# Optimization experiments

Measured on AMD Instinct MI355X. Metric: run time of the kernel, lower is better.

## Reference

```python
import jax, jax.numpy as jnp
import numpy as np

MASS, CHARGE, ALPHA, BETA = 1.0, 0.5, 0.1, 0.05
ETA = jnp.array([1.0, -1.0, -1.0, -1.0], dtype=jnp.float32)  # Minkowski metric diag


def setup_inputs() -> dict:
    key = jax.random.key(0)
    k1, k2, k3 = jax.random.split(key, 3)
    B = 262144
    y = jax.random.normal(k1, (B, 8), dtype=jnp.float32)
    W = jax.random.normal(k2, (4, 4), dtype=jnp.float32) * 0.3
    V = jax.random.normal(k3, (4, 4), dtype=jnp.float32) * 0.3
    return {"y": y, "W": W, "V": V}


def _lagrangian(z):
    # z = (x, u, A) concatenated, shape [12]
    x, u, A = z[0:4], z[4:8], z[8:12]
    kinetic = 0.5 * MASS * jnp.sum(ETA * u * u)
    coupling = CHARGE * jnp.sum(ETA * u * A)
    xu_term = ALPHA * jnp.sum((x * u) ** 2)      # makes J_xu nontrivial
    uA_term = BETA * jnp.sum(u * A) ** 2          # makes J_Au nontrivial
    return kinetic + coupling + xu_term + uA_term


def reference(y, W, V):
    def A_vec(x):  # vector potential A^mu(x), works on [4] or [B,4]
        return jnp.tanh(x @ W.T) + x @ V.T

    x = y[:, 0:4]   # [B,4] positions
    u = y[:, 4:8]   # [B,4] velocities
    A = A_vec(x)    # [B,4]
    z = jnp.concatenate([x, u, A], axis=1)  # [B,12] = (x,u,A)

    gradL = jax.vmap(jax.grad(_lagrangian))(z)      # [B,12]
    H = jax.vmap(jax.hessian(_lagrangian))(z)       # [B,12,12]

    dL_dx = gradL[:, 0:4]
    dL_dA = gradL[:, 8:12]
    J_xu = H[:, 0:4, 4:8]    # d^2L/(dx^mu du^nu)
    J_uu = H[:, 4:8, 4:8]    # d^2L/(du^mu du^nu)
    J_Au = H[:, 8:12, 4:8]   # d^2L/(dA^mu du^nu)

    # dA_dx[a, nu, i] = dA^i/dx^nu (matches tf.stack(..., axis=2) layout)
    jacA = jax.vmap(jax.jacfwd(A_vec))(x)           # [B, i, nu]
    dA_dx = jnp.transpose(jacA, (0, 2, 1))          # [B, nu, i]

    J_uu_inv = jnp.linalg.pinv(J_uu)                # [B,4,4]

    force = (dL_dx
             + jnp.einsum('ajk,ak->aj', dA_dx, dL_dA)
             - jnp.einsum('ai,aij->aj', u,
                          J_xu + jnp.einsum('ajk,akm->ajm', dA_dx, J_Au)))
    acceleration = jnp.einsum('ai,aij->aj', force, J_uu_inv)  # [B,4]
    return acceleration
```

## Files before the change

### kernel.cpp

```cpp
#include <hip/hip_runtime.h>
#include <math.h>


#define SIX_RCOND 2.86102294921875e-5
#define RCOND     4.76837158203125e-6

__device__ __forceinline__ float rcp_nr(float x) {
    float r = __builtin_amdgcn_rcpf(x);
    r = r * (2.0f - x * r);
    return r;
}

__device__ __forceinline__ void fast_tanh4(const double t[4], double th[4])
{
    const double LOG2E = 1.4426950408889634074;
    const double LN2HI = 6.93147180369123816490e-01;
    const double LN2LO = 1.90821492927058770002e-10;
    double e[4], opp[4];
    #pragma unroll
    for (int j = 0; j < 4; ++j) {
        double a  = fabs(t[j]);
        double z  = -2.0 * a;
        double zc = fmax(z, -64.0);
        double nf = rint(zc * LOG2E);
        double r  = fma(-nf, LN2HI, zc);
        r = fma(-nf, LN2LO, r);
        double p = 2.75573192239858906526e-07;
        p = fma(p, r, 2.75573192239858925110e-06);
        p = fma(p, r, 2.48015873015873015873e-05);
        p = fma(p, r, 1.98412698412698412698e-04);
        p = fma(p, r, 1.38888888888888888889e-03);
        p = fma(p, r, 8.33333333333333333333e-03);
        p = fma(p, r, 4.16666666666666666667e-02);
        p = fma(p, r, 1.66666666666666666667e-01);
        p = fma(p, r, 0.5);
        p = fma(p, r, 1.0);
        p = fma(p, r, 1.0);
        int n = (int)nf;
        double twon = __longlong_as_double(((long long)(1023 + n)) << 52);
        double ez = p * twon;
        ez = (z <= -40.0) ? 0.0 : ez;
        e[j]   = ez;
        opp[j] = 1.0 + ez;
    }
    double p01 = opp[0] * opp[1], p23 = opp[2] * opp[3];
    double rp  = 1.0 / (p01 * p23);
    double inv[4] = { opp[1] * p23 * rp, opp[0] * p23 * rp,
                      p01 * opp[3] * rp, p01 * opp[2] * rp };
    #pragma unroll
    for (int j = 0; j < 4; ++j)
        th[j] = copysign((1.0 - e[j]) * inv[j], t[j]);
}

__device__ __forceinline__ void model_terms_f64(
    const double* sW, const double* sV,
    const double x[4], const double u[4],
    double A[4], double f[4], double d[4])
{
    const double eta[4] = {1.0, -1.0, -1.0, -1.0};
    const double CHG = 0.5, ALPHA = 0.1, BETA = 0.05;
    double t[4], s[4];
    #pragma unroll
    for (int j = 0; j < 4; ++j) {
        double tj = 0.0, sj = 0.0;
        #pragma unroll
        for (int k = 0; k < 4; ++k) {
            tj = fma(sW[j*4+k], x[k], tj);
            sj = fma(sV[j*4+k], x[k], sj);
        }
        t[j] = tj; s[j] = sj;
    }
    double th[4];
    fast_tanh4(t, th);
    double G[4][4];
    #pragma unroll
    for (int j = 0; j < 4; ++j) {
        A[j] = th[j] + s[j];
        double dth = 1.0 - th[j] * th[j];
        #pragma unroll
        for (int k = 0; k < 4; ++k) G[j][k] = fma(dth, sW[j*4+k], sV[j*4+k]);
    }
    double S = 0.0;
    #pragma unroll
    for (int k = 0; k < 4; ++k) S += u[k] * A[k];
    double P[4], R[4], Q[4];
    #pragma unroll
    for (int j = 0; j < 4; ++j) {
        double p = 0.0, r = 0.0, q = 0.0;
        #pragma unroll
        for (int k = 0; k < 4; ++k) {
            p += G[k][j] * u[k];
            r += G[j][k] * u[k];
            q += G[k][j] * (CHG * eta[k]) * u[k];
        }
        P[j] = p; R[j] = r; Q[j] = q;
    }
    double T = 0.0;
    #pragma unroll
    for (int j = 0; j < 4; ++j) T += u[j] * R[j];
    #pragma unroll
    for (int j = 0; j < 4; ++j) {
        f[j] = -2.0 * ALPHA * x[j] * u[j] * u[j]
             + Q[j]
             + 2.0 * BETA * S * P[j]
             - (CHG * eta[j] + 2.0 * BETA * S) * R[j]
             - 2.0 * BETA * A[j] * T;
        d[j] = eta[j] + 2.0 * ALPHA * x[j] * x[j];
    }
}

__device__ __forceinline__ void sm_solve_f64(
    const double d[4], const double A[4], const double f[4], double acc[4])
{
    const double C2 = 0.1;
    double b[4], fd[4], den = 1.0, w = 0.0;
    #pragma unroll
    for (int j = 0; j < 4; ++j) {
        double inv = 1.0 / d[j];
        b[j]  = A[j] * inv;
        fd[j] = f[j] * inv;
        den  += C2 * A[j] * b[j];
        w    += b[j] * f[j];
    }
    double scale = C2 * w / den;
    #pragma unroll
    for (int j = 0; j < 4; ++j) acc[j] = fd[j] - b[j] * scale;
}

__device__ __forceinline__ void jacobi_pinv_solve(
    const double d[4], const double A[4], const double f[4], double acc[4])
{
    const double C2 = 0.1;
    double M[4][4], Vm[4][4];
    #pragma unroll
    for (int r = 0; r < 4; ++r) {
        #pragma unroll
        for (int c = 0; c < 4; ++c) {
            M[r][c] = C2 * A[r] * A[c];
            Vm[r][c] = (r == c) ? 1.0 : 0.0;
        }
        M[r][r] += d[r];
    }
    for (int sweep = 0; sweep < 8; ++sweep) {
        #pragma unroll
        for (int p = 0; p < 3; ++p) {
            #pragma unroll
            for (int q2 = p + 1; q2 < 4; ++q2) {
                double apq = M[p][q2];
                bool active = fabs(apq) > 1e-280;
                double div = active ? (2.0 * apq) : 1.0;
                double tau = (M[q2][q2] - M[p][p]) / div;
                double tt = ((tau >= 0.0) ? 1.0 : -1.0) /
                            (fabs(tau) + sqrt(1.0 + tau * tau));
                double c = 1.0 / sqrt(1.0 + tt * tt);
                double s = tt * c;
                c = active ? c : 1.0;
                s = active ? s : 0.0;
                #pragma unroll
                for (int k = 0; k < 4; ++k) {
                    double mkp = M[k][p], mkq = M[k][q2];
                    M[k][p]  = c * mkp - s * mkq;
                    M[k][q2] = s * mkp + c * mkq;
                }
                #pragma unroll
                for (int k = 0; k < 4; ++k) {
                    double mpk = M[p][k], mqk = M[q2][k];
                    M[p][k]  = c * mpk - s * mqk;
                    M[q2][k] = s * mpk + c * mqk;
                }
                #pragma unroll
                for (int k = 0; k < 4; ++k) {
                    double vkp = Vm[k][p], vkq = Vm[k][q2];
                    Vm[k][p]  = c * vkp - s * vkq;
                    Vm[k][q2] = s * vkp + c * vkq;
                }
            }
        }
    }
    double lam[4], sigmax = 0.0;
    #pragma unroll
    for (int k = 0; k < 4; ++k) {
        lam[k] = M[k][k];
        double a = fabs(lam[k]);
        sigmax = (a > sigmax) ? a : sigmax;
    }
    double cutoff = RCOND * sigmax;
    #pragma unroll
    for (int j = 0; j < 4; ++j) acc[j] = 0.0;
    #pragma unroll
    for (int e = 0; e < 4; ++e) {
        double coef = 0.0;
        #pragma unroll
        for (int k = 0; k < 4; ++k) coef += Vm[k][e] * f[k];
        coef /= lam[e];
        coef = (fabs(lam[e]) > cutoff) ? coef : 0.0;
        #pragma unroll
        for (int j = 0; j < 4; ++j) acc[j] += coef * Vm[j][e];
    }
}

__global__ __launch_bounds__(256) void fast_kernel(
    const float* __restrict__ y, const float* __restrict__ W,
    const float* __restrict__ V, float* __restrict__ out,
    unsigned int* __restrict__ cnt, int* __restrict__ list,
    unsigned int cap, int B)
{
    __shared__ float sW[16], sV[16];
    if (threadIdx.x < 16)      sW[threadIdx.x]      = W[threadIdx.x];
    else if (threadIdx.x < 32) sV[threadIdx.x - 16] = V[threadIdx.x - 16];
    __syncthreads();

    int i = blockIdx.x * blockDim.x + threadIdx.x;
    if (i >= B) return;

    const float4* y4 = (const float4*)y;
    float4 xv = y4[2 * i];
    float4 uv = y4[2 * i + 1];
    float x[4] = {xv.x, xv.y, xv.z, xv.w};
    float u[4] = {uv.x, uv.y, uv.z, uv.w};

    const float eta[4] = {1.0f, -1.0f, -1.0f, -1.0f};
    const float CHG = 0.5f, ALPHA = 0.1f, BETA = 0.05f, C2 = 0.1f;
    const float NEG2LOG2E = -2.8853900817779268f;

    float t[4], sv[4];
    #pragma unroll
    for (int j = 0; j < 4; ++j) {
        float tj = 0.0f, sj = 0.0f;
        #pragma unroll
        for (int k = 0; k < 4; ++k) {
            tj = fmaf(sW[j*4+k], x[k], tj);
            sj = fmaf(sV[j*4+k], x[k], sj);
        }
        t[j] = tj; sv[j] = sj;
    }
    float A[4], dth[4];
    #pragma unroll
    for (int j = 0; j < 4; ++j) {
        float a  = fabsf(t[j]);
        float e  = __builtin_amdgcn_exp2f(a * NEG2LOG2E);
        float th = copysignf((1.0f - e) * rcp_nr(1.0f + e), t[j]);
        A[j]   = th + sv[j];
        dth[j] = 1.0f - th * th;
    }
    float G[4][4];
    #pragma unroll
    for (int j = 0; j < 4; ++j)
        #pragma unroll
        for (int k = 0; k < 4; ++k)
            G[j][k] = fmaf(dth[j], sW[j*4+k], sV[j*4+k]);

    float S = 0.0f;
    #pragma unroll
    for (int k = 0; k < 4; ++k) S = fmaf(u[k], A[k], S);
    float P[4], R[4], Q[4];
    #pragma unroll
    for (int j = 0; j < 4; ++j) {
        float p = 0.0f, r = 0.0f, q = 0.0f;
        #pragma unroll
        for (int k = 0; k < 4; ++k) {
            p = fmaf(G[k][j], u[k], p);
            r = fmaf(G[j][k], u[k], r);
            q = fmaf(G[k][j] * (CHG * eta[k]), u[k], q);
        }
        P[j] = p; R[j] = r; Q[j] = q;
    }
    float T = 0.0f;
    #pragma unroll
    for (int j = 0; j < 4; ++j) T = fmaf(u[j], R[j], T);
    float f[4], d[4];
    #pragma unroll
    for (int j = 0; j < 4; ++j) {
        f[j] = -2.0f * ALPHA * x[j] * u[j] * u[j]
             + Q[j]
             + 2.0f * BETA * S * P[j]
             - (CHG * eta[j] + 2.0f * BETA * S) * R[j]
             - 2.0f * BETA * A[j] * T;
        d[j] = eta[j] + 2.0f * ALPHA * x[j] * x[j];
    }

    float mind = fminf(fminf(fabsf(d[0]), fabsf(d[1])),
                       fminf(fabsf(d[2]), fabsf(d[3])));
    float p01 = d[0] * d[1], p23 = d[2] * d[3];
    float prod = p01 * p23;
    float det = prod
        + C2 * (A[0]*A[0]*(d[1]*p23) + A[1]*A[1]*(d[0]*p23) +
                A[2]*A[2]*(p01*d[3]) + A[3]*A[3]*(p01*d[2]));
    float rowmax = 0.0f;
    #pragma unroll
    for (int r = 0; r < 4; ++r) {
        float rs = 0.0f;
        #pragma unroll
        for (int c = 0; c < 4; ++c) {
            float Jrc = C2 * A[r] * A[c] + ((r == c) ? d[r] : 0.0f);
            rs += fabsf(Jrc);
        }
        rowmax = fmaxf(rs, rowmax);
    }
    float sig2 = rowmax * rowmax;
    bool safe = (fabsf(det) > sig2 * sig2 * (1.0f / 1024.0f)) && (mind > 1e-3f);

    if (safe) {
        float invprod = rcp_nr(prod);
        float invd[4] = { d[1] * p23 * invprod, d[0] * p23 * invprod,
                          p01 * d[3] * invprod, p01 * d[2] * invprod };
        float b[4], fd[4], den = 1.0f, w = 0.0f;
        #pragma unroll
        for (int j = 0; j < 4; ++j) {
            b[j]  = A[j] * invd[j];
            fd[j] = f[j] * invd[j];
            den   = fmaf(C2 * A[j], b[j], den);
            w     = fmaf(b[j], f[j], w);
        }
        float scale = (C2 * w) * rcp_nr(den);
        float4 res;
        res.x = fd[0] - b[0] * scale; res.y = fd[1] - b[1] * scale;
        res.z = fd[2] - b[2] * scale; res.w = fd[3] - b[3] * scale;
        ((float4*)out)[i] = res;
    } else {
        unsigned int idx = atomicAdd(cnt, 1u);
        if (idx < cap) {
            list[idx] = i;
        } else {
            float b[4], fd[4], den = 1.0f, w = 0.0f;
            #pragma unroll
            for (int j = 0; j < 4; ++j) {
                float inv = rcp_nr(d[j]);
                b[j]  = A[j] * inv;
                fd[j] = f[j] * inv;
                den   = fmaf(C2 * A[j], b[j], den);
                w     = fmaf(b[j], f[j], w);
            }
            float scale = (C2 * w) * rcp_nr(den);
            float4 res;
            res.x = fd[0] - b[0] * scale; res.y = fd[1] - b[1] * scale;
            res.z = fd[2] - b[2] * scale; res.w = fd[3] - b[3] * scale;
            ((float4*)out)[i] = res;
        }
    }
}

__global__ __launch_bounds__(64, 1) void slow_kernel(
    const float* __restrict__ y, const float* __restrict__ W,
    const float* __restrict__ V, float* __restrict__ out,
    const unsigned int* __restrict__ cnt, const int* __restrict__ list,
    unsigned int cap)
{
    __shared__ double sW[16], sV[16];
    if (threadIdx.x < 16)      sW[threadIdx.x]      = (double)W[threadIdx.x];
    else if (threadIdx.x < 32) sV[threadIdx.x - 16] = (double)V[threadIdx.x - 16];
    __syncthreads();

    unsigned int n = *cnt;
    if (n > cap) n = cap;
    int stride = gridDim.x * blockDim.x;
    for (unsigned int j = blockIdx.x * blockDim.x + threadIdx.x; j < n; j += stride) {
        int i = list[j];
        const float4* y4 = (const float4*)y;
        float4 xv = y4[2 * i];
        float4 uv = y4[2 * i + 1];
        double x[4] = {xv.x, xv.y, xv.z, xv.w};
        double u[4] = {uv.x, uv.y, uv.z, uv.w};
        double A[4], f[4], d[4];
        model_terms_f64(sW, sV, x, u, A, f, d);

        const double C2 = 0.1;
        double mind = 1e300;
        #pragma unroll
        for (int jj = 0; jj < 4; ++jj) {
            double a = fabs(d[jj]);
            mind = (a < mind) ? a : mind;
        }
        double p01 = d[0] * d[1], p23 = d[2] * d[3];
        double det = p01 * p23
            + C2 * (A[0]*A[0]*(d[1]*p23) + A[1]*A[1]*(d[0]*p23) +
                    A[2]*A[2]*(p01*d[3]) + A[3]*A[3]*(p01*d[2]));
        double sumA2 = 0.0, sumA4 = 0.0, F2 = 0.0;
        #pragma unroll
        for (int jj = 0; jj < 4; ++jj) {
            double Aj2 = A[jj] * A[jj];
            sumA2 += Aj2; sumA4 += Aj2 * Aj2;
            double Jjj = d[jj] + C2 * Aj2;
            F2 += Jjj * Jjj;
        }
        F2 += C2 * C2 * (sumA2 * sumA2 - sumA4);
        double rowmax = 0.0;
        #pragma unroll
        for (int r = 0; r < 4; ++r) {
            double rs = 0.0;
            #pragma unroll
            for (int c = 0; c < 4; ++c) {
                double Jrc = C2 * A[r] * A[c] + ((r == c) ? d[r] : 0.0);
                rs += fabs(Jrc);
            }
            rowmax = (rs > rowmax) ? rs : rowmax;
        }
        double sig_hi2 = rowmax * rowmax;
        sig_hi2 = (F2 < sig_hi2) ? F2 : sig_hi2;
        bool safe = (fabs(det) > SIX_RCOND * sig_hi2 * sig_hi2) && (mind > 1e-3);

        double acc[4];
        if (safe) sm_solve_f64(d, A, f, acc);
        else      jacobi_pinv_solve(d, A, f, acc);

        float4 res;
        res.x = (float)acc[0]; res.y = (float)acc[1];
        res.z = (float)acc[2]; res.w = (float)acc[3];
        ((float4*)out)[i] = res;
    }
}

extern "C" void kernel_launch(void* const* d_in, const int* in_sizes, int n_in,
                              void* d_out, int out_size, void* d_ws, size_t ws_size,
                              hipStream_t stream) {
    const float* y = (const float*)d_in[0];
    const float* W = (const float*)d_in[1];
    const float* V = (const float*)d_in[2];
    float* out = (float*)d_out;
    int B = in_sizes[0] / 8;

    unsigned int* cnt = (unsigned int*)d_ws;
    int* list = (int*)((char*)d_ws + 16);
    unsigned int cap = (ws_size > 16) ? (unsigned int)((ws_size - 16) / sizeof(int)) : 0u;
    if (cap > (unsigned int)B) cap = (unsigned int)B;

    hipMemsetAsync(d_ws, 0, 16, stream);

    int block = 256;
    int grid = (B + block - 1) / block;
    fast_kernel<<<grid, block, 0, stream>>>(y, W, V, out, cnt, list, cap, B);
    slow_kernel<<<512, 64, 0, stream>>>(y, W, V, out, cnt, list, cap);
}
```

Measured before the change: 96.27 us.

## Prefilter unsafe rows with f64 criterion in fast kernel, shrink slow-path list

The fast kernel now recomputes model terms in double precision for rows that fail the f32 safety test. It solves them in place with the f64 Sherman-Morrison path when the f64 criterion passes, and only defers truly ill-conditioned rows to the slow kernel. The slow kernel now always runs Jacobi pinv, keeps its eigenvector matrix in LDS to relieve register pressure, and launches half as many blocks. This trades extra f64 work and LDS use in the fast kernel for a smaller slow-path workload and a smaller tail latency.

```diff
diff --git a/kernel.cpp b/kernel.cpp
--- a/kernel.cpp
+++ b/kernel.cpp
@@ -127,17 +127,57 @@
     for (int j = 0; j < 4; ++j) acc[j] = fd[j] - b[j] * scale;
 }
 
-__device__ __forceinline__ void jacobi_pinv_solve(
-    const double d[4], const double A[4], const double f[4], double acc[4])
+__device__ __forceinline__ bool criterion_f64(
+    const double d[4], const double A[4])
 {
     const double C2 = 0.1;
-    double M[4][4], Vm[4][4];
+    double mind = 1e300;
+    #pragma unroll
+    for (int j = 0; j < 4; ++j) {
+        double a = fabs(d[j]);
+        mind = (a < mind) ? a : mind;
+    }
+    double p01 = d[0] * d[1], p23 = d[2] * d[3];
+    double det = p01 * p23
+        + C2 * (A[0]*A[0]*(d[1]*p23) + A[1]*A[1]*(d[0]*p23) +
+                A[2]*A[2]*(p01*d[3]) + A[3]*A[3]*(p01*d[2]));
+    double sumA2 = 0.0, sumA4 = 0.0, F2 = 0.0;
+    #pragma unroll
+    for (int j = 0; j < 4; ++j) {
+        double Aj2 = A[j] * A[j];
+        sumA2 += Aj2; sumA4 += Aj2 * Aj2;
+        double Jjj = d[j] + C2 * Aj2;
+        F2 += Jjj * Jjj;
+    }
+    F2 += C2 * C2 * (sumA2 * sumA2 - sumA4);
+    double rowmax = 0.0;
+    #pragma unroll
+    for (int r = 0; r < 4; ++r) {
+        double rs = 0.0;
+        #pragma unroll
+        for (int c = 0; c < 4; ++c) {
+            double Jrc = C2 * A[r] * A[c] + ((r == c) ? d[r] : 0.0);
+            rs += fabs(Jrc);
+        }
+        rowmax = (rs > rowmax) ? rs : rowmax;
+    }
+    double sig_hi2 = rowmax * rowmax;
+    sig_hi2 = (F2 < sig_hi2) ? F2 : sig_hi2;
+    return (fabs(det) > SIX_RCOND * sig_hi2 * sig_hi2) && (mind > 1e-3);
+}
+
+__device__ __forceinline__ void jacobi_pinv_lds(
+    const double d[4], const double A[4], const double f[4], double acc[4],
+    double* __restrict__ Vm)
+{
+    const double C2 = 0.1;
+    double M[4][4];
     #pragma unroll
     for (int r = 0; r < 4; ++r) {
         #pragma unroll
         for (int c = 0; c < 4; ++c) {
             M[r][c] = C2 * A[r] * A[c];
-            Vm[r][c] = (r == c) ? 1.0 : 0.0;
+            Vm[r*4+c] = (r == c) ? 1.0 : 0.0;
         }
         M[r][r] += d[r];
     }
@@ -170,9 +210,9 @@
                 }
                 #pragma unroll
                 for (int k = 0; k < 4; ++k) {
-                    double vkp = Vm[k][p], vkq = Vm[k][q2];
-                    Vm[k][p]  = c * vkp - s * vkq;
-                    Vm[k][q2] = s * vkp + c * vkq;
+                    double vkp = Vm[k*4+p], vkq = Vm[k*4+q2];
+                    Vm[k*4+p]  = c * vkp - s * vkq;
+                    Vm[k*4+q2] = s * vkp + c * vkq;
                 }
             }
         }
@@ -191,11 +231,11 @@
     for (int e = 0; e < 4; ++e) {
         double coef = 0.0;
         #pragma unroll
-        for (int k = 0; k < 4; ++k) coef += Vm[k][e] * f[k];
+        for (int k = 0; k < 4; ++k) coef += Vm[k*4+e] * f[k];
         coef /= lam[e];
         coef = (fabs(lam[e]) > cutoff) ? coef : 0.0;
         #pragma unroll
-        for (int j = 0; j < 4; ++j) acc[j] += coef * Vm[j][e];
+        for (int j = 0; j < 4; ++j) acc[j] += coef * Vm[j*4+e];
     }
 }
 
@@ -205,9 +245,17 @@
     unsigned int* __restrict__ cnt, int* __restrict__ list,
     unsigned int cap, int B)
 {
-    __shared__ float sW[16], sV[16];
-    if (threadIdx.x < 16)      sW[threadIdx.x]      = W[threadIdx.x];
-    else if (threadIdx.x < 32) sV[threadIdx.x - 16] = V[threadIdx.x - 16];
+    __shared__ float  sW[16],  sV[16];
+    __shared__ double sWd[16], sVd[16];
+    if (threadIdx.x < 16) {
+        float w = W[threadIdx.x];
+        sW[threadIdx.x]  = w;
+        sWd[threadIdx.x] = (double)w;
+    } else if (threadIdx.x < 32) {
+        float v = V[threadIdx.x - 16];
+        sV[threadIdx.x - 16]  = v;
+        sVd[threadIdx.x - 16] = (double)v;
+    }
     __syncthreads();
 
     int i = blockIdx.x * blockDim.x + threadIdx.x;
@@ -318,23 +366,22 @@
         res.z = fd[2] - b[2] * scale; res.w = fd[3] - b[3] * scale;
         ((float4*)out)[i] = res;
     } else {
-        unsigned int idx = atomicAdd(cnt, 1u);
-        if (idx < cap) {
-            list[idx] = i;
-        } else {
-            float b[4], fd[4], den = 1.0f, w = 0.0f;
-            #pragma unroll
-            for (int j = 0; j < 4; ++j) {
-                float inv = rcp_nr(d[j]);
-                b[j]  = A[j] * inv;
-                fd[j] = f[j] * inv;
-                den   = fmaf(C2 * A[j], b[j], den);
-                w     = fmaf(b[j], f[j], w);
-            }
-            float scale = (C2 * w) * rcp_nr(den);
+        double xd[4] = {xv.x, xv.y, xv.z, xv.w};
+        double ud[4] = {uv.x, uv.y, uv.z, uv.w};
+        double Ad[4], fd64[4], dd[4];
+        model_terms_f64(sWd, sVd, xd, ud, Ad, fd64, dd);
+        bool safe64 = criterion_f64(dd, Ad);
+        bool deferred = false;
+        if (!safe64) {
+            unsigned int idx = atomicAdd(cnt, 1u);
+            if (idx < cap) { list[idx] = i; deferred = true; }
+        }
+        if (!deferred) {
+            double acc[4];
+            sm_solve_f64(dd, Ad, fd64, acc);
             float4 res;
-            res.x = fd[0] - b[0] * scale; res.y = fd[1] - b[1] * scale;
-            res.z = fd[2] - b[2] * scale; res.w = fd[3] - b[3] * scale;
+            res.x = (float)acc[0]; res.y = (float)acc[1];
+            res.z = (float)acc[2]; res.w = (float)acc[3];
             ((float4*)out)[i] = res;
         }
     }
@@ -347,6 +394,7 @@
     unsigned int cap)
 {
     __shared__ double sW[16], sV[16];
+    __shared__ double VmL[64][17];
     if (threadIdx.x < 16)      sW[threadIdx.x]      = (double)W[threadIdx.x];
     else if (threadIdx.x < 32) sV[threadIdx.x - 16] = (double)V[threadIdx.x - 16];
     __syncthreads();
@@ -364,44 +412,8 @@
         double A[4], f[4], d[4];
         model_terms_f64(sW, sV, x, u, A, f, d);
 
-        const double C2 = 0.1;
-        double mind = 1e300;
-        #pragma unroll
-        for (int jj = 0; jj < 4; ++jj) {
-            double a = fabs(d[jj]);
-            mind = (a < mind) ? a : mind;
-        }
-        double p01 = d[0] * d[1], p23 = d[2] * d[3];
-        double det = p01 * p23
-            + C2 * (A[0]*A[0]*(d[1]*p23) + A[1]*A[1]*(d[0]*p23) +
-                    A[2]*A[2]*(p01*d[3]) + A[3]*A[3]*(p01*d[2]));
-        double sumA2 = 0.0, sumA4 = 0.0, F2 = 0.0;
-        #pragma unroll
-        for (int jj = 0; jj < 4; ++jj) {
-            double Aj2 = A[jj] * A[jj];
-            sumA2 += Aj2; sumA4 += Aj2 * Aj2;
-            double Jjj = d[jj] + C2 * Aj2;
-            F2 += Jjj * Jjj;
-        }
-        F2 += C2 * C2 * (sumA2 * sumA2 - sumA4);
-        double rowmax = 0.0;
-        #pragma unroll
-        for (int r = 0; r < 4; ++r) {
-            double rs = 0.0;
-            #pragma unroll
-            for (int c = 0; c < 4; ++c) {
-                double Jrc = C2 * A[r] * A[c] + ((r == c) ? d[r] : 0.0);
-                rs += fabs(Jrc);
-            }
-            rowmax = (rs > rowmax) ? rs : rowmax;
-        }
-        double sig_hi2 = rowmax * rowmax;
-        sig_hi2 = (F2 < sig_hi2) ? F2 : sig_hi2;
-        bool safe = (fabs(det) > SIX_RCOND * sig_hi2 * sig_hi2) && (mind > 1e-3);
-
         double acc[4];
-        if (safe) sm_solve_f64(d, A, f, acc);
-        else      jacobi_pinv_solve(d, A, f, acc);
+        jacobi_pinv_lds(d, A, f, acc, VmL[threadIdx.x]);
 
         float4 res;
         res.x = (float)acc[0]; res.y = (float)acc[1];
@@ -429,5 +441,5 @@
     int block = 256;
     int grid = (B + block - 1) / block;
     fast_kernel<<<grid, block, 0, stream>>>(y, W, V, out, cnt, list, cap, B);
-    slow_kernel<<<512, 64, 0, stream>>>(y, W, V, out, cnt, list, cap);
-}
+    slow_kernel<<<256, 64, 0, stream>>>(y, W, V, out, cnt, list, cap);
+}
```

Result: faster. 83.88 us (-12.9%).
